# Optimization experiments

Measured on AMD Instinct MI355X. Metric: run time of the kernel, lower is better.

Reference implementation:

```python
import jax, jax.numpy as jnp
import numpy as np

HID, SD, EXP, DTR = 1024, 16, 2048, 64
B_, T_ = 4, 2048


def setup_inputs() -> dict:
    key = jax.random.key(0)
    ks = jax.random.split(key, 9)
    def rn(k, shape, s=0.02):
        return jax.random.normal(k, shape, jnp.float32) * s
    return {
        "x": jax.random.normal(ks[0], (B_, T_, HID), jnp.float32),
        "ln_g": jnp.ones((HID,), jnp.float32),
        "ln_b": jnp.zeros((HID,), jnp.float32),
        "W_in": rn(ks[1], (HID, 2 * EXP)),
        "b_in": jnp.zeros((2 * EXP,), jnp.float32),
        "W_del": rn(ks[2], (EXP, DTR)),
        "b_del": jnp.zeros((DTR,), jnp.float32),
        "W_dt": rn(ks[3], (DTR, EXP)),
        "b_dt": jnp.zeros((EXP,), jnp.float32),
        "W_B": rn(ks[4], (EXP, SD)),
        "b_B": jnp.zeros((SD,), jnp.float32),
        "W_C": rn(ks[5], (EXP, SD)),
        "b_C": jnp.zeros((SD,), jnp.float32),
        "A_log": -jnp.exp(0.1 * jax.random.normal(ks[6], (EXP, SD), jnp.float32)),
        "Dp": jnp.zeros((EXP,), jnp.float32),
        "W_out": rn(ks[7], (EXP, HID)),
        "b_out": jnp.zeros((HID,), jnp.float32),
    }


def _layernorm(x, g, b, eps=1e-5):
    m = jnp.mean(x, axis=-1, keepdims=True)
    v = jnp.var(x, axis=-1, keepdims=True)
    return (x - m) * jax.lax.rsqrt(v + eps) * g + b


def _selective_scan(u, delta, A, Bm, Cm):
    # u, delta: (B,T,E); Bm, Cm: (B,T,Sd); A: (E,Sd)
    def step(h, inp):
        u_t, d_t, B_t, C_t = inp  # (B,E),(B,E),(B,Sd),(B,Sd)
        A_disc = jnp.exp(d_t[..., None] * A[None])          # (B,E,Sd)
        h = A_disc * h + d_t[..., None] * B_t[:, None, :] * u_t[..., None]
        y_t = jnp.einsum("bs,bds->bd", C_t, h)
        return h, y_t
    h0 = jnp.zeros((u.shape[0], u.shape[2], A.shape[1]), u.dtype)
    xs = (u.transpose(1, 0, 2), delta.transpose(1, 0, 2),
          Bm.transpose(1, 0, 2), Cm.transpose(1, 0, 2))
    _, ys = jax.lax.scan(step, h0, xs)  # ys: (T,B,E)
    return ys.transpose(1, 0, 2)


def reference(x, ln_g, ln_b, W_in, b_in, W_del, b_del, W_dt, b_dt,
              W_B, b_B, W_C, b_C, A_log, Dp, W_out, b_out):
    res = x
    xn = _layernorm(x, ln_g, ln_b)
    xp = xn @ W_in + b_in                 # (B,T,2E)
    u, gate = jnp.split(xp, 2, axis=-1)   # each (B,T,E)
    u = jax.nn.silu(u)
    delta = jax.nn.softplus((u @ W_del + b_del) @ W_dt + b_dt)  # (B,T,E)
    Bm = u @ W_B + b_B                    # (B,T,Sd)
    Cm = u @ W_C + b_C                    # (B,T,Sd)
    A = -jnp.exp(A_log)                   # (E,Sd)
    y = _selective_scan(u, delta, A, Bm, Cm)
    y = y + u * Dp
    y = y * jax.nn.silu(gate)
    return y @ W_out + b_out + res
```

## Files before the change

### kernel.cpp

```cpp
#include <hip/hip_runtime.h>

#define HIDN 1024
#define EXPN 2048
#define SDIM 16
#define DTRN 64
#define BBN  4
#define TTN  2048
#define MMN  (BBN*TTN)
#define NCHUNK 32
#define CLEN (TTN/NCHUNK)
#define KSPL 8
#define KCH  (EXPN/KSPL)

typedef unsigned short u16;
typedef __bf16 bf16x8 __attribute__((ext_vector_type(8)));
typedef float f32x4 __attribute__((ext_vector_type(4)));

static __device__ __forceinline__ float b2f(u16 u) {
    union { unsigned int i; float f; } cv; cv.i = ((unsigned int)u) << 16; return cv.f;
}
static __device__ __forceinline__ u16 f2b(float f) {
    union { float f; unsigned int i; } cv; cv.f = f;
    unsigned int x = cv.i;
    return (u16)((x + 0x7fffu + ((x >> 16) & 1u)) >> 16);
}
static __device__ __forceinline__ float fexp2(float x) {
    return __builtin_amdgcn_exp2f(x);
}
static __device__ __forceinline__ float fsilu(float v) {
    return v / (1.f + fexp2(-1.44269504088896f * v));
}

static __device__ __forceinline__
void tr_tile(const float* __restrict__ W, u16* __restrict__ Wt,
             int K, int N, int bk, int bn, float (*t)[65]) {
    const int r0 = threadIdx.x >> 4, c0 = (threadIdx.x & 15) << 2;
    #pragma unroll
    for (int i = 0; i < 4; ++i) {
        float4 v = *(const float4*)(W + (size_t)(bk + r0 + i * 16) * N + bn + c0);
        t[r0 + i * 16][c0 + 0] = v.x; t[r0 + i * 16][c0 + 1] = v.y;
        t[r0 + i * 16][c0 + 2] = v.z; t[r0 + i * 16][c0 + 3] = v.w;
    }
    __syncthreads();
    #pragma unroll
    for (int i = 0; i < 4; ++i) {
        const int n = r0 + i * 16;
        ushort4 o;
        o.x = f2b(t[c0 + 0][n]); o.y = f2b(t[c0 + 1][n]);
        o.z = f2b(t[c0 + 2][n]); o.w = f2b(t[c0 + 3][n]);
        *(ushort4*)(Wt + (size_t)(bn + n) * K + bk + c0) = o;
    }
}

__global__ __launch_bounds__(256)
void k_prep(const float* __restrict__ W_in, const float* __restrict__ W_out,
            const float* __restrict__ W_dt, const float* __restrict__ W_del,
            const float* __restrict__ W_B, const float* __restrict__ W_C,
            const float* __restrict__ A_log,
            u16* __restrict__ Wt_in, u16* __restrict__ Wt_out,
            u16* __restrict__ Wdt_t, u16* __restrict__ Wcat,
            float* __restrict__ A2) {
    __shared__ float t[64][65];
    int blk = blockIdx.x;
    if (blk < 1024) {
        tr_tile(W_in, Wt_in, HIDN, 2 * EXPN, (blk >> 6) << 6, (blk & 63) << 6, t);
        return;
    }
    blk -= 1024;
    if (blk < 512) {
        tr_tile(W_out, Wt_out, EXPN, HIDN, (blk >> 4) << 6, (blk & 15) << 6, t);
        return;
    }
    blk -= 512;
    if (blk < 32) {
        tr_tile(W_dt, Wdt_t, DTRN, EXPN, 0, blk << 6, t);
        return;
    }
    blk -= 32;
    if (blk < 768) {
        const int i = blk * 256 + threadIdx.x;
        const int n = i >> 11, k = i & 2047;
        float v;
        if (n < 64)      v = W_del[(size_t)k * DTRN + n];
        else if (n < 80) v = W_B[(size_t)k * SDIM + (n - 64)];
        else             v = W_C[(size_t)k * SDIM + (n - 80)];
        Wcat[i] = f2b(v);
        return;
    }
    blk -= 768;
    {
        const int i = blk * 256 + threadIdx.x;
        A2[i] = -__expf(A_log[i]) * 1.44269504088896340736f;
    }
}

__global__ __launch_bounds__(256) void k_ln(const float* __restrict__ x,
                                            const float* __restrict__ g,
                                            const float* __restrict__ bta,
                                            u16* __restrict__ xn) {
    const int row = blockIdx.x, tid = threadIdx.x;
    const float4 xv = ((const float4*)(x + (size_t)row * HIDN))[tid];
    float s  = xv.x + xv.y + xv.z + xv.w;
    float ss = fmaf(xv.x, xv.x, fmaf(xv.y, xv.y, fmaf(xv.z, xv.z, xv.w * xv.w)));
    #pragma unroll
    for (int o = 32; o > 0; o >>= 1) { s += __shfl_down(s, o); ss += __shfl_down(ss, o); }
    __shared__ float as[4], bs[4];
    const int wid = tid >> 6, lane = tid & 63;
    if (lane == 0) { as[wid] = s; bs[wid] = ss; }
    __syncthreads();
    const float S  = as[0] + as[1] + as[2] + as[3];
    const float SS = bs[0] + bs[1] + bs[2] + bs[3];
    const float mean = S * (1.f / HIDN);
    const float var  = SS * (1.f / HIDN) - mean * mean;
    const float r = rsqrtf(var + 1e-5f);
    const float4 gv = ((const float4*)g)[tid];
    const float4 bv = ((const float4*)bta)[tid];
    ushort4 o;
    o.x = f2b((xv.x - mean) * r * gv.x + bv.x);
    o.y = f2b((xv.y - mean) * r * gv.y + bv.y);
    o.z = f2b((xv.z - mean) * r * gv.z + bv.z);
    o.w = f2b((xv.w - mean) * r * gv.w + bv.w);
    ((ushort4*)(xn + (size_t)row * HIDN))[tid] = o;
}

#define MEPI_SPLIT_SILU 0
#define MEPI_OUT        1
#define MEPI_SP         2

static __device__ __forceinline__
void stage256(const u16* __restrict__ A, const u16* __restrict__ Bt,
              u16 (*seg)[8192], int brow, int bcol, int K, int k0,
              int srow, int scol, int tid) {
    #pragma unroll
    for (int h = 0; h < 2; ++h) {
        const u16* sa = A + (size_t)(brow + h * 128 + srow) * K + k0 + scol;
        __builtin_amdgcn_global_load_lds(
            (const __attribute__((address_space(1))) void*)sa,
            (__attribute__((address_space(3))) void*)&seg[h][tid * 8], 16, 0, 0);
        const u16* sb = Bt + (size_t)(bcol + h * 128 + srow) * K + k0 + scol;
        __builtin_amdgcn_global_load_lds(
            (const __attribute__((address_space(1))) void*)sb,
            (__attribute__((address_space(3))) void*)&seg[2 + h][tid * 8], 16, 0, 0);
    }
}

template<int EPI>
__global__ __launch_bounds__(1024)
void mgemm256(const u16* __restrict__ A, const u16* __restrict__ Bt,
              const float* __restrict__ bias, void* __restrict__ O0,
              void* __restrict__ O1, const float* __restrict__ res,
              int N, int K) {
    __shared__ u16 lds[2][4][8192];
    const int tid  = threadIdx.x;
    const int lane = tid & 63, wid = tid >> 6;
    const int wm = wid >> 2, wn = wid & 3;
    const int r  = lane & 15, kh = lane >> 4;
    const int brow = blockIdx.y * 256, bcol = blockIdx.x * 256;

    int srow, scol;
    {
        const int q = tid;
        const int sub = q >> 6, qi = q & 63;
        const int qis = qi ^ (((qi >> 5) & 1) << 1);
        srow = (sub >> 1) * 16 + (qi >> 2);
        scol = ((sub & 1) << 5) + (qis & 3) * 8;
    }
    const int swz_kh = kh ^ (((r >> 3) & 1) << 1);
    const int rbase  = r * 32 + swz_kh * 8;
    const int am = wm & 1, bq = wn & 1;

    f32x4 acc[4][4];
    #pragma unroll
    for (int i = 0; i < 4; ++i)
        #pragma unroll
        for (int n = 0; n < 4; ++n) acc[i][n] = (f32x4){0.f, 0.f, 0.f, 0.f};

    const int NT = K >> 6;
    stage256(A, Bt, lds[0], brow, bcol, K, 0, srow, scol, tid);
    stage256(A, Bt, lds[1], brow, bcol, K, 64, srow, scol, tid);
    asm volatile("s_waitcnt vmcnt(4)" ::: "memory");
    __builtin_amdgcn_s_barrier();
    asm volatile("" ::: "memory");

    for (int kt = 0; kt < NT; ++kt) {
        const u16* segA = lds[kt & 1][wm >> 1];
        const u16* segB = lds[kt & 1][2 + (wn >> 1)];
        #pragma unroll
        for (int kk = 0; kk < 2; ++kk) {
            bf16x8 a[4], b[4];
            #pragma unroll
            for (int mf = 0; mf < 4; ++mf)
                a[mf] = *(const bf16x8*)&segA[((am * 4 + mf) * 2 + kk) * 512 + rbase];
            #pragma unroll
            for (int nf = 0; nf < 4; ++nf)
                b[nf] = *(const bf16x8*)&segB[((bq * 4 + nf) * 2 + kk) * 512 + rbase];
            __builtin_amdgcn_s_setprio(1);
            #pragma unroll
            for (int mf = 0; mf < 4; ++mf)
                #pragma unroll
                for (int nf = 0; nf < 4; ++nf)
                    acc[mf][nf] = __builtin_amdgcn_mfma_f32_16x16x32_bf16(a[mf], b[nf], acc[mf][nf], 0, 0, 0);
            __builtin_amdgcn_s_setprio(0);
        }
        __builtin_amdgcn_s_barrier(); asm volatile("" ::: "memory");
        if (kt + 2 < NT) {
            stage256(A, Bt, lds[kt & 1], brow, bcol, K, (kt + 2) * 64, srow, scol, tid);
            asm volatile("s_waitcnt vmcnt(4)" ::: "memory");
        } else {
            asm volatile("s_waitcnt vmcnt(0)" ::: "memory");
        }
        __builtin_amdgcn_s_barrier(); asm volatile("" ::: "memory");
    }

    const int orow = brow + wm * 64 + kh * 4;
    const int ocol = bcol + wn * 64 + r;
    if constexpr (EPI == MEPI_SPLIT_SILU) {
        u16* dst; int cb;
        if (bcol < EXPN) { dst = (u16*)O0; cb = ocol; }
        else             { dst = (u16*)O1; cb = ocol - EXPN; }
        #pragma unroll
        for (int Mf = 0; Mf < 4; ++Mf)
            #pragma unroll
            for (int Nf = 0; Nf < 4; ++Nf)
                #pragma unroll
                for (int j = 0; j < 4; ++j) {
                    const int row = orow + Mf * 16 + j;
                    const int col = ocol + Nf * 16;
                    float v = acc[Mf][Nf][j] + bias[col];
                    dst[(size_t)row * EXPN + cb + Nf * 16] = f2b(fsilu(v));
                }
    } else {
        float* o = (float*)O0;
        #pragma unroll
        for (int Mf = 0; Mf < 4; ++Mf)
            #pragma unroll
            for (int Nf = 0; Nf < 4; ++Nf)
                #pragma unroll
                for (int j = 0; j < 4; ++j) {
                    const int row = orow + Mf * 16 + j;
                    const int col = ocol + Nf * 16;
                    o[(size_t)row * N + col] = acc[Mf][Nf][j] + bias[col] + res[(size_t)row * N + col];
                }
    }
}

template<int EPI>
__global__ __launch_bounds__(256)
void mgemm(const u16* __restrict__ A, const u16* __restrict__ Bt,
           const float* __restrict__ bias, void* __restrict__ O0,
           void* __restrict__ O1, const float* __restrict__ res,
           int N, int K) {
    __shared__ u16 As[128 * 32];
    __shared__ u16 Bs[128 * 32];
    const int tid  = threadIdx.x;
    const int wave = tid >> 6, lane = tid & 63;
    const int brow = blockIdx.y * 128, bcol = blockIdx.x * 128;
    const int wm = wave >> 1, wn = wave & 1;
    const int r  = lane & 15, kh = lane >> 4;

    f32x4 acc[4][4];
    #pragma unroll
    for (int m = 0; m < 4; m++)
        #pragma unroll
        for (int n = 0; n < 4; n++) acc[m][n] = (f32x4){0.f, 0.f, 0.f, 0.f};

    const u16* ga0 = A  + (size_t)(brow +      (tid >> 2)) * K + (tid & 3) * 8;
    const u16* ga1 = A  + (size_t)(brow + 64 + (tid >> 2)) * K + (tid & 3) * 8;
    const u16* gb0 = Bt + (size_t)(bcol +      (tid >> 2)) * K + (tid & 3) * 8;
    const u16* gb1 = Bt + (size_t)(bcol + 64 + (tid >> 2)) * K + (tid & 3) * 8;
    u16* lA0 = As + (wave * 64) * 8;
    u16* lA1 = As + (256 + wave * 64) * 8;
    u16* lB0 = Bs + (wave * 64) * 8;
    u16* lB1 = Bs + (256 + wave * 64) * 8;

    for (int k0 = 0; k0 < K; k0 += 32) {
        __syncthreads();
        __builtin_amdgcn_global_load_lds((const __attribute__((address_space(1))) void*)(ga0 + k0),
                                         (__attribute__((address_space(3))) void*)lA0, 16, 0, 0);
        __builtin_amdgcn_global_load_lds((const __attribute__((address_space(1))) void*)(ga1 + k0),
                                         (__attribute__((address_space(3))) void*)lA1, 16, 0, 0);
        __builtin_amdgcn_global_load_lds((const __attribute__((address_space(1))) void*)(gb0 + k0),
                                         (__attribute__((address_space(3))) void*)lB0, 16, 0, 0);
        __builtin_amdgcn_global_load_lds((const __attribute__((address_space(1))) void*)(gb1 + k0),
                                         (__attribute__((address_space(3))) void*)lB1, 16, 0, 0);
        __syncthreads();
        bf16x8 af[4], bfr[4];
        #pragma unroll
        for (int mf = 0; mf < 4; ++mf)
            af[mf] = *(const bf16x8*)(As + ((wm * 64 + mf * 16 + r) * 32 + kh * 8));
        #pragma unroll
        for (int nf = 0; nf < 4; ++nf)
            bfr[nf] = *(const bf16x8*)(Bs + ((wn * 64 + nf * 16 + r) * 32 + kh * 8));
        #pragma unroll
        for (int mf = 0; mf < 4; ++mf)
            #pragma unroll
            for (int nf = 0; nf < 4; ++nf)
                acc[mf][nf] = __builtin_amdgcn_mfma_f32_16x16x32_bf16(af[mf], bfr[nf], acc[mf][nf], 0, 0, 0);
    }

    const int orow = brow + wm * 64 + kh * 4;
    const int ocol = bcol + wn * 64 + r;
    if constexpr (EPI == MEPI_SP) {
        u16* o = (u16*)O0;
        #pragma unroll
        for (int mf = 0; mf < 4; ++mf)
            #pragma unroll
            for (int nf = 0; nf < 4; ++nf)
                #pragma unroll
                for (int j = 0; j < 4; ++j) {
                    const int row = orow + mf * 16 + j;
                    const int col = ocol + nf * 16;
                    float v = acc[mf][nf][j] + bias[col];
                    float sp = (v > 20.f) ? v
                             : 0.69314718056f * __builtin_amdgcn_logf(
                                   1.f + fexp2(1.44269504089f * v));
                    o[(size_t)row * N + col] = f2b(sp);
                }
    } else {
        float* o = (float*)O0;
        #pragma unroll
        for (int mf = 0; mf < 4; ++mf)
            #pragma unroll
            for (int nf = 0; nf < 4; ++nf)
                #pragma unroll
                for (int j = 0; j < 4; ++j) {
                    const int row = orow + mf * 16 + j;
                    const int col = ocol + nf * 16;
                    o[(size_t)row * N + col] = acc[mf][nf][j] + bias[col] + res[(size_t)row * N + col];
                }
    }
}

__global__ __launch_bounds__(256)
void k_proj(const u16* __restrict__ A, const u16* __restrict__ Wcat,
            float* __restrict__ Ppart) {
    __shared__ u16 As[128 * 32];
    __shared__ u16 Bs[96 * 32];
    const int tid  = threadIdx.x;
    const int wave = tid >> 6, lane = tid & 63;
    const int brow = blockIdx.y * 128;
    const int ks   = blockIdx.x;
    const int r = lane & 15, kh = lane >> 4;

    f32x4 acc[2][6];
    #pragma unroll
    for (int m = 0; m < 2; m++)
        #pragma unroll
        for (int n = 0; n < 6; n++) acc[m][n] = (f32x4){0.f, 0.f, 0.f, 0.f};

    const u16* ga0 = A + (size_t)(brow +      (tid >> 2)) * EXPN + ks * KCH + (tid & 3) * 8;
    const u16* ga1 = A + (size_t)(brow + 64 + (tid >> 2)) * EXPN + ks * KCH + (tid & 3) * 8;
    const u16* gb0 = Wcat + (size_t)(tid >> 2) * EXPN + ks * KCH + (tid & 3) * 8;
    const u16* gb1 = Wcat + (size_t)(64 + (tid >> 2)) * EXPN + ks * KCH + (tid & 3) * 8;
    u16* lA0 = As + (wave * 64) * 8;
    u16* lA1 = As + (256 + wave * 64) * 8;
    u16* lB0 = Bs + (wave * 64) * 8;
    u16* lB1 = Bs + (256 + wave * 64) * 8;

    for (int k0 = 0; k0 < KCH; k0 += 32) {
        __syncthreads();
        __builtin_amdgcn_global_load_lds((const __attribute__((address_space(1))) void*)(ga0 + k0),
                                         (__attribute__((address_space(3))) void*)lA0, 16, 0, 0);
        __builtin_amdgcn_global_load_lds((const __attribute__((address_space(1))) void*)(ga1 + k0),
                                         (__attribute__((address_space(3))) void*)lA1, 16, 0, 0);
        __builtin_amdgcn_global_load_lds((const __attribute__((address_space(1))) void*)(gb0 + k0),
                                         (__attribute__((address_space(3))) void*)lB0, 16, 0, 0);
        if (tid < 128)
            __builtin_amdgcn_global_load_lds((const __attribute__((address_space(1))) void*)(gb1 + k0),
                                             (__attribute__((address_space(3))) void*)lB1, 16, 0, 0);
        __syncthreads();
        bf16x8 af[2], bfr[6];
        #pragma unroll
        for (int mf = 0; mf < 2; ++mf)
            af[mf] = *(const bf16x8*)(As + ((wave * 32 + mf * 16 + r) * 32 + kh * 8));
        #pragma unroll
        for (int nf = 0; nf < 6; ++nf)
            bfr[nf] = *(const bf16x8*)(Bs + ((nf * 16 + r) * 32 + kh * 8));
        #pragma unroll
        for (int mf = 0; mf < 2; ++mf)
            #pragma unroll
            for (int nf = 0; nf < 6; ++nf)
                acc[mf][nf] = __builtin_amdgcn_mfma_f32_16x16x32_bf16(af[mf], bfr[nf], acc[mf][nf], 0, 0, 0);
    }
    const int orow = brow + wave * 32 + kh * 4;
    #pragma unroll
    for (int mf = 0; mf < 2; ++mf)
        #pragma unroll
        for (int nf = 0; nf < 6; ++nf)
            #pragma unroll
            for (int j = 0; j < 4; ++j)
                Ppart[((size_t)ks * MMN + orow + mf * 16 + j) * 96 + nf * 16 + r] = acc[mf][nf][j];
}

__global__ __launch_bounds__(192)
void k_red(const float* __restrict__ Ppart, const float* __restrict__ b_del,
           const float* __restrict__ b_B, const float* __restrict__ b_C,
           u16* __restrict__ t1b, float* __restrict__ Bm, float* __restrict__ Cm) {
    const int tid = threadIdx.x;
    const int ri  = tid / 96, col = tid - ri * 96;
    const int row = blockIdx.x * 2 + ri;
    float s = 0.f;
    #pragma unroll
    for (int ks = 0; ks < KSPL; ++ks)
        s += Ppart[((size_t)ks * MMN + row) * 96 + col];
    if (col < 64)      t1b[(size_t)row * DTRN + col] = f2b(s + b_del[col]);
    else if (col < 80) Bm[(size_t)row * SDIM + col - 64] = s + b_B[col - 64];
    else               Cm[(size_t)row * SDIM + col - 80] = s + b_C[col - 80];
}

__global__ __launch_bounds__(256)
void k_scan1(const u16* __restrict__ ub, const u16* __restrict__ db,
             const float* __restrict__ Bm, const float* __restrict__ A2,
             float* __restrict__ hend, float* __restrict__ Pp) {
    const int e = blockIdx.x * 256 + threadIdx.x;
    const int c = blockIdx.y, b = blockIdx.z;
    float a2[SDIM], h[SDIM];
    {
        const float4* ap = (const float4*)(A2 + (size_t)e * SDIM);
        float4 v0 = ap[0], v1 = ap[1], v2 = ap[2], v3 = ap[3];
        a2[0]=v0.x; a2[1]=v0.y; a2[2]=v0.z; a2[3]=v0.w;
        a2[4]=v1.x; a2[5]=v1.y; a2[6]=v1.z; a2[7]=v1.w;
        a2[8]=v2.x; a2[9]=v2.y; a2[10]=v2.z; a2[11]=v2.w;
        a2[12]=v3.x; a2[13]=v3.y; a2[14]=v3.z; a2[15]=v3.w;
    }
    #pragma unroll
    for (int s = 0; s < SDIM; s++) h[s] = 0.f;
    float sumd = 0.f;
    const int t0 = c * CLEN;
    size_t rb = ((size_t)b * TTN + t0) * EXPN + e;
    size_t bb_ = ((size_t)b * TTN + t0) * SDIM;
    for (int tt = 0; tt < CLEN; ++tt) {
        const float d  = b2f(db[rb]);
        const float uv = b2f(ub[rb]);
        const float4* bp = (const float4*)(Bm + bb_);
        float4 b0 = bp[0], b1 = bp[1], b2v = bp[2], b3 = bp[3];
        float bv[SDIM] = { b0.x,b0.y,b0.z,b0.w, b1.x,b1.y,b1.z,b1.w,
                           b2v.x,b2v.y,b2v.z,b2v.w, b3.x,b3.y,b3.z,b3.w };
        const float du = d * uv;
        sumd += d;
        #pragma unroll
        for (int s = 0; s < SDIM; ++s) {
            float ad = fexp2(d * a2[s]);
            h[s] = fmaf(ad, h[s], du * bv[s]);
        }
        rb += EXPN; bb_ += SDIM;
    }
    size_t ob = ((size_t)(b * NCHUNK + c) * SDIM) * EXPN + e;
    #pragma unroll
    for (int s = 0; s < SDIM; ++s) {
        hend[ob + (size_t)s * EXPN] = h[s];
        Pp  [ob + (size_t)s * EXPN] = fexp2(a2[s] * sumd);
    }
}

__global__ __launch_bounds__(256)
void k_fix(const float* __restrict__ hend, const float* __restrict__ Pp,
           float* __restrict__ hinit) {
    const int i = blockIdx.x * 256 + threadIdx.x;
    const int b = blockIdx.y;
    float hi = 0.f;
    size_t base = ((size_t)b * NCHUNK) * SDIM * EXPN + i;
    for (int cc = 0; cc < NCHUNK; ++cc) {
        size_t idx = base + (size_t)cc * SDIM * EXPN;
        hinit[idx] = hi;
        hi = fmaf(Pp[idx], hi, hend[idx]);
    }
}

__global__ __launch_bounds__(256)
void k_scan2(const u16* __restrict__ ub, const u16* __restrict__ db,
             const u16* __restrict__ sgb, const float* __restrict__ Bm,
             const float* __restrict__ Cm, const float* __restrict__ A2,
             const float* __restrict__ hinit, const float* __restrict__ Dp,
             u16* __restrict__ yb) {
    const int e = blockIdx.x * 256 + threadIdx.x;
    const int c = blockIdx.y, b = blockIdx.z;
    float a2[SDIM], h[SDIM];
    {
        const float4* ap = (const float4*)(A2 + (size_t)e * SDIM);
        float4 v0 = ap[0], v1 = ap[1], v2 = ap[2], v3 = ap[3];
        a2[0]=v0.x; a2[1]=v0.y; a2[2]=v0.z; a2[3]=v0.w;
        a2[4]=v1.x; a2[5]=v1.y; a2[6]=v1.z; a2[7]=v1.w;
        a2[8]=v2.x; a2[9]=v2.y; a2[10]=v2.z; a2[11]=v2.w;
        a2[12]=v3.x; a2[13]=v3.y; a2[14]=v3.z; a2[15]=v3.w;
    }
    {
        size_t hb = ((size_t)(b * NCHUNK + c) * SDIM) * EXPN + e;
        #pragma unroll
        for (int s = 0; s < SDIM; s++) h[s] = hinit[hb + (size_t)s * EXPN];
    }
    const float dpe = Dp[e];
    const int t0 = c * CLEN;
    size_t rb = ((size_t)b * TTN + t0) * EXPN + e;
    size_t bb_ = ((size_t)b * TTN + t0) * SDIM;
    for (int tt = 0; tt < CLEN; ++tt) {
        const float d   = b2f(db[rb]);
        const float uv  = b2f(ub[rb]);
        const float sgv = b2f(sgb[rb]);
        const float4* bp = (const float4*)(Bm + bb_);
        const float4* cp = (const float4*)(Cm + bb_);
        float4 b0 = bp[0], b1 = bp[1], b2v = bp[2], b3 = bp[3];
        float4 c0 = cp[0], c1 = cp[1], c2v = cp[2], c3 = cp[3];
        float bv[SDIM] = { b0.x,b0.y,b0.z,b0.w, b1.x,b1.y,b1.z,b1.w,
                           b2v.x,b2v.y,b2v.z,b2v.w, b3.x,b3.y,b3.z,b3.w };
        float cv[SDIM] = { c0.x,c0.y,c0.z,c0.w, c1.x,c1.y,c1.z,c1.w,
                           c2v.x,c2v.y,c2v.z,c2v.w, c3.x,c3.y,c3.z,c3.w };
        const float du = d * uv;
        float yt = 0.f;
        #pragma unroll
        for (int s = 0; s < SDIM; ++s) {
            float ad = fexp2(d * a2[s]);
            h[s] = fmaf(ad, h[s], du * bv[s]);
            yt = fmaf(cv[s], h[s], yt);
        }
        yb[rb] = f2b(fmaf(uv, dpe, yt) * sgv);
        rb += EXPN; bb_ += SDIM;
    }
}

extern "C" void kernel_launch(void* const* d_in, const int* in_sizes, int n_in,
                              void* d_out, int out_size, void* d_ws, size_t ws_size,
                              hipStream_t stream) {
    const float* x     = (const float*)d_in[0];
    const float* ln_g  = (const float*)d_in[1];
    const float* ln_b  = (const float*)d_in[2];
    const float* W_in  = (const float*)d_in[3];
    const float* b_in  = (const float*)d_in[4];
    const float* W_del = (const float*)d_in[5];
    const float* b_del = (const float*)d_in[6];
    const float* W_dt  = (const float*)d_in[7];
    const float* b_dt  = (const float*)d_in[8];
    const float* W_B   = (const float*)d_in[9];
    const float* b_B   = (const float*)d_in[10];
    const float* W_C   = (const float*)d_in[11];
    const float* b_C   = (const float*)d_in[12];
    const float* A_log = (const float*)d_in[13];
    const float* Dp    = (const float*)d_in[14];
    const float* W_out = (const float*)d_in[15];
    const float* b_out = (const float*)d_in[16];
    float* out = (float*)d_out;

    char* p = (char*)d_ws;
    auto alloc = [&](size_t bytes) {
        char* r = p; p += (bytes + 255) & ~(size_t)255; return (void*)r;
    };
    u16* xn   = (u16*)alloc((size_t)MMN * HIDN * 2);
    u16* u    = (u16*)alloc((size_t)MMN * EXPN * 2);
    u16* sg   = (u16*)alloc((size_t)MMN * EXPN * 2);
    u16* dl   = (u16*)alloc((size_t)MMN * EXPN * 2);
    u16* y    = (u16*)alloc((size_t)MMN * EXPN * 2);
    u16* t1b  = (u16*)alloc((size_t)MMN * DTRN * 2);
    float* Bm = (float*)alloc((size_t)MMN * SDIM * 4);
    float* Cm = (float*)alloc((size_t)MMN * SDIM * 4);
    float* A2 = (float*)alloc((size_t)EXPN * SDIM * 4);
    u16* Wt_in  = (u16*)alloc((size_t)(2 * EXPN) * HIDN * 2);
    u16* Wt_out = (u16*)alloc((size_t)HIDN * EXPN * 2);
    u16* Wcat   = (u16*)alloc((size_t)96 * EXPN * 2);
    u16* Wdt_t  = (u16*)alloc((size_t)EXPN * DTRN * 2);
    const size_t hsz = (size_t)BBN * NCHUNK * EXPN * SDIM * 4;
    float* hend  = (float*)alloc(hsz);
    float* Pp    = (float*)alloc(hsz);
    float* hinit = (float*)alloc(hsz);
    float* Ppart = hend;

    k_prep<<<dim3(1024 + 512 + 32 + 768 + 128), 256, 0, stream>>>(
        W_in, W_out, W_dt, W_del, W_B, W_C, A_log, Wt_in, Wt_out, Wdt_t, Wcat, A2);
    k_ln<<<dim3(MMN), 256, 0, stream>>>(x, ln_g, ln_b, xn);

    mgemm256<MEPI_SPLIT_SILU><<<dim3(2 * EXPN / 256, MMN / 256), 1024, 0, stream>>>(
        xn, Wt_in, b_in, u, sg, nullptr, 2 * EXPN, HIDN);
    k_proj<<<dim3(KSPL, MMN / 128), 256, 0, stream>>>(u, Wcat, Ppart);
    k_red<<<dim3(MMN / 2), 192, 0, stream>>>(Ppart, b_del, b_B, b_C, t1b, Bm, Cm);
    mgemm<MEPI_SP><<<dim3(EXPN / 128, MMN / 128), 256, 0, stream>>>(
        t1b, Wdt_t, b_dt, dl, nullptr, nullptr, EXPN, DTRN);
    k_scan1<<<dim3(EXPN / 256, NCHUNK, BBN), 256, 0, stream>>>(u, dl, Bm, A2, hend, Pp);
    k_fix<<<dim3(SDIM * EXPN / 256, BBN), 256, 0, stream>>>(hend, Pp, hinit);
    k_scan2<<<dim3(EXPN / 256, NCHUNK, BBN), 256, 0, stream>>>(u, dl, sg, Bm, Cm, A2, hinit, Dp, y);
    mgemm<MEPI_OUT><<<dim3(HIDN / 128, MMN / 128), 256, 0, stream>>>(
        y, Wt_out, b_out, out, nullptr, x, HIDN, EXPN);
}
```

Baseline: 302.6 us.

## Generalize 256-row pipelined GEMM over BN and use it for dt and out projections

Templates the 1024-thread double-buffered global_load_lds GEMM on the tile width BN (256 or 128). It replaces the older 128x128 single-buffered GEMM used for the softplus delta projection and the output projection, so those now get swizzled LDS, prefetch depth two and larger 256x128 tiles. It also merges the layernorm kernel into the weight-prep launch to save one kernel launch. The larger tiles halve the block count for the out projection (256 blocks), which may lower occupancy and SM fill, and the K=64 dt GEMM takes a new single-tile path.

```diff
diff --git a/kernel.cpp b/kernel.cpp
--- a/kernel.cpp
+++ b/kernel.cpp
@@ -30,6 +30,11 @@
 static __device__ __forceinline__ float fsilu(float v) {
     return v / (1.f + fexp2(-1.44269504088896f * v));
 }
+template<int L> static __device__ __forceinline__ void waitcnt_vm() {
+    if constexpr (L == 0) asm volatile("s_waitcnt vmcnt(0)" ::: "memory");
+    else if constexpr (L == 3) asm volatile("s_waitcnt vmcnt(3)" ::: "memory");
+    else if constexpr (L == 4) asm volatile("s_waitcnt vmcnt(4)" ::: "memory");
+}
 
 static __device__ __forceinline__
 void tr_tile(const float* __restrict__ W, u16* __restrict__ Wt,
@@ -53,15 +58,45 @@
 }
 
 __global__ __launch_bounds__(256)
-void k_prep(const float* __restrict__ W_in, const float* __restrict__ W_out,
+void k_prep(const float* __restrict__ x, const float* __restrict__ ln_g,
+            const float* __restrict__ ln_b,
+            const float* __restrict__ W_in, const float* __restrict__ W_out,
             const float* __restrict__ W_dt, const float* __restrict__ W_del,
             const float* __restrict__ W_B, const float* __restrict__ W_C,
             const float* __restrict__ A_log,
+            u16* __restrict__ xn,
             u16* __restrict__ Wt_in, u16* __restrict__ Wt_out,
             u16* __restrict__ Wdt_t, u16* __restrict__ Wcat,
             float* __restrict__ A2) {
     __shared__ float t[64][65];
+    __shared__ float as[4], bs[4];
     int blk = blockIdx.x;
+    if (blk < MMN) {
+        const int row = blk, tid = threadIdx.x;
+        const float4 xv = ((const float4*)(x + (size_t)row * HIDN))[tid];
+        float s  = xv.x + xv.y + xv.z + xv.w;
+        float ss = fmaf(xv.x, xv.x, fmaf(xv.y, xv.y, fmaf(xv.z, xv.z, xv.w * xv.w)));
+        #pragma unroll
+        for (int o = 32; o > 0; o >>= 1) { s += __shfl_down(s, o); ss += __shfl_down(ss, o); }
+        const int wid = tid >> 6, lane = tid & 63;
+        if (lane == 0) { as[wid] = s; bs[wid] = ss; }
+        __syncthreads();
+        const float S  = as[0] + as[1] + as[2] + as[3];
+        const float SS = bs[0] + bs[1] + bs[2] + bs[3];
+        const float mean = S * (1.f / HIDN);
+        const float var  = SS * (1.f / HIDN) - mean * mean;
+        const float r = rsqrtf(var + 1e-5f);
+        const float4 gv = ((const float4*)ln_g)[tid];
+        const float4 bv = ((const float4*)ln_b)[tid];
+        ushort4 o;
+        o.x = f2b((xv.x - mean) * r * gv.x + bv.x);
+        o.y = f2b((xv.y - mean) * r * gv.y + bv.y);
+        o.z = f2b((xv.z - mean) * r * gv.z + bv.z);
+        o.w = f2b((xv.w - mean) * r * gv.w + bv.w);
+        ((ushort4*)(xn + (size_t)row * HIDN))[tid] = o;
+        return;
+    }
+    blk -= MMN;
     if (blk < 1024) {
         tr_tile(W_in, Wt_in, HIDN, 2 * EXPN, (blk >> 6) << 6, (blk & 63) << 6, t);
         return;
@@ -94,39 +129,11 @@
     }
 }
 
-__global__ __launch_bounds__(256) void k_ln(const float* __restrict__ x,
-                                            const float* __restrict__ g,
-                                            const float* __restrict__ bta,
-                                            u16* __restrict__ xn) {
-    const int row = blockIdx.x, tid = threadIdx.x;
-    const float4 xv = ((const float4*)(x + (size_t)row * HIDN))[tid];
-    float s  = xv.x + xv.y + xv.z + xv.w;
-    float ss = fmaf(xv.x, xv.x, fmaf(xv.y, xv.y, fmaf(xv.z, xv.z, xv.w * xv.w)));
-    #pragma unroll
-    for (int o = 32; o > 0; o >>= 1) { s += __shfl_down(s, o); ss += __shfl_down(ss, o); }
-    __shared__ float as[4], bs[4];
-    const int wid = tid >> 6, lane = tid & 63;
-    if (lane == 0) { as[wid] = s; bs[wid] = ss; }
-    __syncthreads();
-    const float S  = as[0] + as[1] + as[2] + as[3];
-    const float SS = bs[0] + bs[1] + bs[2] + bs[3];
-    const float mean = S * (1.f / HIDN);
-    const float var  = SS * (1.f / HIDN) - mean * mean;
-    const float r = rsqrtf(var + 1e-5f);
-    const float4 gv = ((const float4*)g)[tid];
-    const float4 bv = ((const float4*)bta)[tid];
-    ushort4 o;
-    o.x = f2b((xv.x - mean) * r * gv.x + bv.x);
-    o.y = f2b((xv.y - mean) * r * gv.y + bv.y);
-    o.z = f2b((xv.z - mean) * r * gv.z + bv.z);
-    o.w = f2b((xv.w - mean) * r * gv.w + bv.w);
-    ((ushort4*)(xn + (size_t)row * HIDN))[tid] = o;
-}
-
 #define MEPI_SPLIT_SILU 0
 #define MEPI_OUT        1
 #define MEPI_SP         2
 
+template<int BN>
 static __device__ __forceinline__
 void stage256(const u16* __restrict__ A, const u16* __restrict__ Bt,
               u16 (*seg)[8192], int brow, int bcol, int K, int k0,
@@ -137,6 +144,9 @@
         __builtin_amdgcn_global_load_lds(
             (const __attribute__((address_space(1))) void*)sa,
             (__attribute__((address_space(3))) void*)&seg[h][tid * 8], 16, 0, 0);
+    }
+    #pragma unroll
+    for (int h = 0; h < BN / 128; ++h) {
         const u16* sb = Bt + (size_t)(bcol + h * 128 + srow) * K + k0 + scol;
         __builtin_amdgcn_global_load_lds(
             (const __attribute__((address_space(1))) void*)sb,
@@ -144,18 +154,22 @@
     }
 }
 
-template<int EPI>
+template<int BN, int EPI>
 __global__ __launch_bounds__(1024)
 void mgemm256(const u16* __restrict__ A, const u16* __restrict__ Bt,
               const float* __restrict__ bias, void* __restrict__ O0,
               void* __restrict__ O1, const float* __restrict__ res,
               int N, int K) {
-    __shared__ u16 lds[2][4][8192];
+    constexpr int NSEG = 2 + BN / 128;
+    constexpr int L    = NSEG;
+    constexpr int NF   = BN / 64 / 4 * 4 / 4;
+    constexpr int NFRag = BN / 64;
+    __shared__ u16 lds[2][NSEG][8192];
     const int tid  = threadIdx.x;
     const int lane = tid & 63, wid = tid >> 6;
     const int wm = wid >> 2, wn = wid & 3;
     const int r  = lane & 15, kh = lane >> 4;
-    const int brow = blockIdx.y * 256, bcol = blockIdx.x * 256;
+    const int brow = blockIdx.y * 256, bcol = blockIdx.x * BN;
 
     int srow, scol;
     {
@@ -167,53 +181,59 @@
     }
     const int swz_kh = kh ^ (((r >> 3) & 1) << 1);
     const int rbase  = r * 32 + swz_kh * 8;
-    const int am = wm & 1, bq = wn & 1;
-
-    f32x4 acc[4][4];
+    const int am = wm & 1;
+
+    f32x4 acc[4][NFRag];
     #pragma unroll
     for (int i = 0; i < 4; ++i)
         #pragma unroll
-        for (int n = 0; n < 4; ++n) acc[i][n] = (f32x4){0.f, 0.f, 0.f, 0.f};
+        for (int n = 0; n < NFRag; ++n) acc[i][n] = (f32x4){0.f, 0.f, 0.f, 0.f};
 
     const int NT = K >> 6;
-    stage256(A, Bt, lds[0], brow, bcol, K, 0, srow, scol, tid);
-    stage256(A, Bt, lds[1], brow, bcol, K, 64, srow, scol, tid);
-    asm volatile("s_waitcnt vmcnt(4)" ::: "memory");
+    stage256<BN>(A, Bt, lds[0], brow, bcol, K, 0, srow, scol, tid);
+    if (NT > 1) {
+        stage256<BN>(A, Bt, lds[1], brow, bcol, K, 64, srow, scol, tid);
+        waitcnt_vm<L>();
+    } else {
+        waitcnt_vm<0>();
+    }
     __builtin_amdgcn_s_barrier();
     asm volatile("" ::: "memory");
 
     for (int kt = 0; kt < NT; ++kt) {
         const u16* segA = lds[kt & 1][wm >> 1];
-        const u16* segB = lds[kt & 1][2 + (wn >> 1)];
         #pragma unroll
         for (int kk = 0; kk < 2; ++kk) {
-            bf16x8 a[4], b[4];
+            bf16x8 a[4], b[NFRag];
             #pragma unroll
             for (int mf = 0; mf < 4; ++mf)
                 a[mf] = *(const bf16x8*)&segA[((am * 4 + mf) * 2 + kk) * 512 + rbase];
             #pragma unroll
-            for (int nf = 0; nf < 4; ++nf)
-                b[nf] = *(const bf16x8*)&segB[((bq * 4 + nf) * 2 + kk) * 512 + rbase];
+            for (int nf = 0; nf < NFRag; ++nf) {
+                const int nb = wn * NFRag + nf;
+                const u16* segB = lds[kt & 1][2 + (nb >> 3)];
+                b[nf] = *(const bf16x8*)&segB[(((nb & 7)) * 2 + kk) * 512 + rbase];
+            }
             __builtin_amdgcn_s_setprio(1);
             #pragma unroll
             for (int mf = 0; mf < 4; ++mf)
                 #pragma unroll
-                for (int nf = 0; nf < 4; ++nf)
+                for (int nf = 0; nf < NFRag; ++nf)
                     acc[mf][nf] = __builtin_amdgcn_mfma_f32_16x16x32_bf16(a[mf], b[nf], acc[mf][nf], 0, 0, 0);
             __builtin_amdgcn_s_setprio(0);
         }
         __builtin_amdgcn_s_barrier(); asm volatile("" ::: "memory");
         if (kt + 2 < NT) {
-            stage256(A, Bt, lds[kt & 1], brow, bcol, K, (kt + 2) * 64, srow, scol, tid);
-            asm volatile("s_waitcnt vmcnt(4)" ::: "memory");
+            stage256<BN>(A, Bt, lds[kt & 1], brow, bcol, K, (kt + 2) * 64, srow, scol, tid);
+            waitcnt_vm<L>();
         } else {
-            asm volatile("s_waitcnt vmcnt(0)" ::: "memory");
+            waitcnt_vm<0>();
         }
         __builtin_amdgcn_s_barrier(); asm volatile("" ::: "memory");
     }
 
     const int orow = brow + wm * 64 + kh * 4;
-    const int ocol = bcol + wn * 64 + r;
+    const int ocol = bcol + wn * (BN / 4) + r;
     if constexpr (EPI == MEPI_SPLIT_SILU) {
         u16* dst; int cb;
         if (bcol < EXPN) { dst = (u16*)O0; cb = ocol; }
@@ -221,7 +241,7 @@
         #pragma unroll
         for (int Mf = 0; Mf < 4; ++Mf)
             #pragma unroll
-            for (int Nf = 0; Nf < 4; ++Nf)
+            for (int Nf = 0; Nf < NFRag; ++Nf)
                 #pragma unroll
                 for (int j = 0; j < 4; ++j) {
                     const int row = orow + Mf * 16 + j;
@@ -229,88 +249,17 @@
                     float v = acc[Mf][Nf][j] + bias[col];
                     dst[(size_t)row * EXPN + cb + Nf * 16] = f2b(fsilu(v));
                 }
-    } else {
-        float* o = (float*)O0;
+    } else if constexpr (EPI == MEPI_SP) {
+        u16* o = (u16*)O0;
         #pragma unroll
         for (int Mf = 0; Mf < 4; ++Mf)
             #pragma unroll
-            for (int Nf = 0; Nf < 4; ++Nf)
+            for (int Nf = 0; Nf < NFRag; ++Nf)
                 #pragma unroll
                 for (int j = 0; j < 4; ++j) {
                     const int row = orow + Mf * 16 + j;
                     const int col = ocol + Nf * 16;
-                    o[(size_t)row * N + col] = acc[Mf][Nf][j] + bias[col] + res[(size_t)row * N + col];
-                }
-    }
-}
-
-template<int EPI>
-__global__ __launch_bounds__(256)
-void mgemm(const u16* __restrict__ A, const u16* __restrict__ Bt,
-           const float* __restrict__ bias, void* __restrict__ O0,
-           void* __restrict__ O1, const float* __restrict__ res,
-           int N, int K) {
-    __shared__ u16 As[128 * 32];
-    __shared__ u16 Bs[128 * 32];
-    const int tid  = threadIdx.x;
-    const int wave = tid >> 6, lane = tid & 63;
-    const int brow = blockIdx.y * 128, bcol = blockIdx.x * 128;
-    const int wm = wave >> 1, wn = wave & 1;
-    const int r  = lane & 15, kh = lane >> 4;
-
-    f32x4 acc[4][4];
-    #pragma unroll
-    for (int m = 0; m < 4; m++)
-        #pragma unroll
-        for (int n = 0; n < 4; n++) acc[m][n] = (f32x4){0.f, 0.f, 0.f, 0.f};
-
-    const u16* ga0 = A  + (size_t)(brow +      (tid >> 2)) * K + (tid & 3) * 8;
-    const u16* ga1 = A  + (size_t)(brow + 64 + (tid >> 2)) * K + (tid & 3) * 8;
-    const u16* gb0 = Bt + (size_t)(bcol +      (tid >> 2)) * K + (tid & 3) * 8;
-    const u16* gb1 = Bt + (size_t)(bcol + 64 + (tid >> 2)) * K + (tid & 3) * 8;
-    u16* lA0 = As + (wave * 64) * 8;
-    u16* lA1 = As + (256 + wave * 64) * 8;
-    u16* lB0 = Bs + (wave * 64) * 8;
-    u16* lB1 = Bs + (256 + wave * 64) * 8;
-
-    for (int k0 = 0; k0 < K; k0 += 32) {
-        __syncthreads();
-        __builtin_amdgcn_global_load_lds((const __attribute__((address_space(1))) void*)(ga0 + k0),
-                                         (__attribute__((address_space(3))) void*)lA0, 16, 0, 0);
-        __builtin_amdgcn_global_load_lds((const __attribute__((address_space(1))) void*)(ga1 + k0),
-                                         (__attribute__((address_space(3))) void*)lA1, 16, 0, 0);
-        __builtin_amdgcn_global_load_lds((const __attribute__((address_space(1))) void*)(gb0 + k0),
-                                         (__attribute__((address_space(3))) void*)lB0, 16, 0, 0);
-        __builtin_amdgcn_global_load_lds((const __attribute__((address_space(1))) void*)(gb1 + k0),
-                                         (__attribute__((address_space(3))) void*)lB1, 16, 0, 0);
-        __syncthreads();
-        bf16x8 af[4], bfr[4];
-        #pragma unroll
-        for (int mf = 0; mf < 4; ++mf)
-            af[mf] = *(const bf16x8*)(As + ((wm * 64 + mf * 16 + r) * 32 + kh * 8));
-        #pragma unroll
-        for (int nf = 0; nf < 4; ++nf)
-            bfr[nf] = *(const bf16x8*)(Bs + ((wn * 64 + nf * 16 + r) * 32 + kh * 8));
-        #pragma unroll
-        for (int mf = 0; mf < 4; ++mf)
-            #pragma unroll
-            for (int nf = 0; nf < 4; ++nf)
-                acc[mf][nf] = __builtin_amdgcn_mfma_f32_16x16x32_bf16(af[mf], bfr[nf], acc[mf][nf], 0, 0, 0);
-    }
-
-    const int orow = brow + wm * 64 + kh * 4;
-    const int ocol = bcol + wn * 64 + r;
-    if constexpr (EPI == MEPI_SP) {
-        u16* o = (u16*)O0;
-        #pragma unroll
-        for (int mf = 0; mf < 4; ++mf)
-            #pragma unroll
-            for (int nf = 0; nf < 4; ++nf)
-                #pragma unroll
-                for (int j = 0; j < 4; ++j) {
-                    const int row = orow + mf * 16 + j;
-                    const int col = ocol + nf * 16;
-                    float v = acc[mf][nf][j] + bias[col];
+                    float v = acc[Mf][Nf][j] + bias[col];
                     float sp = (v > 20.f) ? v
                              : 0.69314718056f * __builtin_amdgcn_logf(
                                    1.f + fexp2(1.44269504089f * v));
@@ -319,14 +268,14 @@
     } else {
         float* o = (float*)O0;
         #pragma unroll
-        for (int mf = 0; mf < 4; ++mf)
-            #pragma unroll
-            for (int nf = 0; nf < 4; ++nf)
+        for (int Mf = 0; Mf < 4; ++Mf)
+            #pragma unroll
+            for (int Nf = 0; Nf < NFRag; ++Nf)
                 #pragma unroll
                 for (int j = 0; j < 4; ++j) {
-                    const int row = orow + mf * 16 + j;
-                    const int col = ocol + nf * 16;
-                    o[(size_t)row * N + col] = acc[mf][nf][j] + bias[col] + res[(size_t)row * N + col];
+                    const int row = orow + Mf * 16 + j;
+                    const int col = ocol + Nf * 16;
+                    o[(size_t)row * N + col] = acc[Mf][Nf][j] + bias[col] + res[(size_t)row * N + col];
                 }
     }
 }
@@ -563,19 +512,19 @@
     float* hinit = (float*)alloc(hsz);
     float* Ppart = hend;
 
-    k_prep<<<dim3(1024 + 512 + 32 + 768 + 128), 256, 0, stream>>>(
-        W_in, W_out, W_dt, W_del, W_B, W_C, A_log, Wt_in, Wt_out, Wdt_t, Wcat, A2);
-    k_ln<<<dim3(MMN), 256, 0, stream>>>(x, ln_g, ln_b, xn);
-
-    mgemm256<MEPI_SPLIT_SILU><<<dim3(2 * EXPN / 256, MMN / 256), 1024, 0, stream>>>(
+    k_prep<<<dim3(MMN + 1024 + 512 + 32 + 768 + 128), 256, 0, stream>>>(
+        x, ln_g, ln_b, W_in, W_out, W_dt, W_del, W_B, W_C, A_log,
+        xn, Wt_in, Wt_out, Wdt_t, Wcat, A2);
+
+    mgemm256<256, MEPI_SPLIT_SILU><<<dim3(2 * EXPN / 256, MMN / 256), 1024, 0, stream>>>(
         xn, Wt_in, b_in, u, sg, nullptr, 2 * EXPN, HIDN);
     k_proj<<<dim3(KSPL, MMN / 128), 256, 0, stream>>>(u, Wcat, Ppart);
     k_red<<<dim3(MMN / 2), 192, 0, stream>>>(Ppart, b_del, b_B, b_C, t1b, Bm, Cm);
-    mgemm<MEPI_SP><<<dim3(EXPN / 128, MMN / 128), 256, 0, stream>>>(
+    mgemm256<128, MEPI_SP><<<dim3(EXPN / 128, MMN / 256), 1024, 0, stream>>>(
         t1b, Wdt_t, b_dt, dl, nullptr, nullptr, EXPN, DTRN);
     k_scan1<<<dim3(EXPN / 256, NCHUNK, BBN), 256, 0, stream>>>(u, dl, Bm, A2, hend, Pp);
     k_fix<<<dim3(SDIM * EXPN / 256, BBN), 256, 0, stream>>>(hend, Pp, hinit);
     k_scan2<<<dim3(EXPN / 256, NCHUNK, BBN), 256, 0, stream>>>(u, dl, sg, Bm, Cm, A2, hinit, Dp, y);
-    mgemm<MEPI_OUT><<<dim3(HIDN / 128, MMN / 128), 256, 0, stream>>>(
+    mgemm256<128, MEPI_OUT><<<dim3(HIDN / 128, MMN / 256), 1024, 0, stream>>>(
         y, Wt_out, b_out, out, nullptr, x, HIDN, EXPN);
 }
```

After: 294.2 us. -2.8%, faster.
